# Optimization experiments

Hardware: AMD Instinct MI355X
Metric: run time of the kernel (lower is better)

Reference implementation:

```python
import jax, jax.numpy as jnp
import numpy as np
import math

N_HEADS = 16
D_KV = 64
NUM_BUCKETS = 32
MAX_DISTANCE = 128


def _rel_bucket(rel_pos, num_buckets=NUM_BUCKETS, max_distance=MAX_DISTANCE):
    # bidirectional=True branch of relative_position_bucket
    n = -rel_pos
    num_buckets //= 2
    ret = (n < 0).astype(jnp.int32) * num_buckets
    n = jnp.abs(n)
    max_exact = num_buckets // 2
    is_small = n < max_exact
    val_large = max_exact + (
        jnp.log(n.astype(jnp.float32) / max_exact)
        / math.log(max_distance / max_exact)
        * (num_buckets - max_exact)
    ).astype(jnp.int32)
    val_large = jnp.minimum(val_large, num_buckets - 1)
    return jnp.where(is_small, n, val_large) + ret


def setup_inputs() -> dict:
    key = jax.random.key(0)
    ks = jax.random.split(key, 6)
    T, D = 2048, 1024
    x = jax.random.normal(ks[0], (T, D), dtype=jnp.float32)
    Wq = jax.random.normal(ks[1], (D, N_HEADS * D_KV), dtype=jnp.float32) * 0.02
    Wk = jax.random.normal(ks[2], (D, N_HEADS * D_KV), dtype=jnp.float32) * 0.02
    Wv = jax.random.normal(ks[3], (D, N_HEADS * D_KV), dtype=jnp.float32) * 0.02
    Wo = jax.random.normal(ks[4], (N_HEADS * D_KV, D), dtype=jnp.float32) * 0.02
    rel_bias_table = jax.random.normal(ks[5], (NUM_BUCKETS, N_HEADS), dtype=jnp.float32) * 0.02
    q_lens = jnp.full((4,), 512, dtype=jnp.int32)  # packed varlen: 4 seqs of 512, sum == T
    return {"x": x, "Wq": Wq, "Wk": Wk, "Wv": Wv, "Wo": Wo,
            "rel_bias_table": rel_bias_table, "q_lens": q_lens}


def _attention(x, Wq, Wk, Wv, Wo, rel_bias_table, q_lens):
    T = x.shape[0]
    q = x @ Wq
    k = x @ Wk
    v = x @ Wv
    to_heads = lambda t: jnp.transpose(t.reshape(T, N_HEADS, D_KV), (1, 0, 2))  # [H,T,d]
    q_h, k_h, v_h = to_heads(q), to_heads(k), to_heads(v)

    # fp32 scores (no 1/sqrt(d) scaling in T5; module uses scaling=1.0)
    scores = jnp.einsum('hqd,hkd->hqk', q_h.astype(jnp.float32), k_h.astype(jnp.float32))

    # sequence ids / positions within packed layout
    starts = jnp.cumsum(q_lens, dtype=jnp.int32) - q_lens
    indicators = jnp.zeros(T, dtype=jnp.int32).at[starts].set(1)
    seq_ids = jnp.cumsum(indicators, dtype=jnp.int32) - 1
    pos = jnp.arange(T) - starts[seq_ids]

    # relative position bias (encoder: bidirectional)
    rel_pos = pos[None, :] - pos[:, None]  # [T,T]
    buckets = _rel_bucket(rel_pos)
    bias = jnp.transpose(rel_bias_table[buckets], (2, 0, 1))  # [H,T,T]
    scores = scores + bias.astype(jnp.float32)

    # block-diagonal mask over packed sequences (non-causal encoder)
    total = jnp.sum(q_lens)
    valid = jnp.arange(T) < total
    mask = (seq_ids[:, None] == seq_ids[None, :]) & valid[:, None] & valid[None, :]
    scores = jnp.where(mask[None], scores, jnp.finfo(scores.dtype).min)

    weights = jax.nn.softmax(scores, axis=-1)
    out = jnp.einsum('hqk,hkd->hqd', weights, v_h.astype(jnp.float32))
    out = jnp.transpose(out, (1, 0, 2)).reshape(T, N_HEADS * D_KV)
    return out.astype(x.dtype) @ Wo


def reference(x, Wq, Wk, Wv, Wo, rel_bias_table, q_lens):
    return _attention(x, Wq, Wk, Wv, Wo, rel_bias_table, q_lens)
```

## Files before the change

### kernel.cpp

```cpp
#include <hip/hip_runtime.h>

#define NH 16

typedef __bf16 bf16x8 __attribute__((ext_vector_type(8)));
typedef unsigned short u16x8 __attribute__((ext_vector_type(8)));
typedef float f32x4 __attribute__((ext_vector_type(4)));
typedef unsigned short u16;

__device__ __forceinline__ u16 f2bu(float f) {
    unsigned int u = __builtin_bit_cast(unsigned int, f);
    u = (u + 0x7FFFu + ((u >> 16) & 1u)) >> 16;
    return (u16)u;
}
__device__ __forceinline__ bf16x8 ld_bf8(const u16* p) {
    return __builtin_bit_cast(bf16x8, *(const u16x8*)p);
}
__device__ __forceinline__ void gl_lds16(const void* g, void* l) {
    __builtin_amdgcn_global_load_lds((const __attribute__((address_space(1))) void*)g,
                                     (__attribute__((address_space(3))) void*)l, 16, 0, 0);
}

__device__ __forceinline__ int rel_bucket(int delta) {
    int n = -delta;
    int ret = (n < 0) ? 16 : 0;
    int na = n < 0 ? -n : n;
    int b;
    if (na < 8) b = na;
    else if (na < 12) b = 8;
    else if (na < 16) b = 9;
    else if (na < 23) b = 10;
    else if (na < 32) b = 11;
    else if (na < 46) b = 12;
    else if (na < 64) b = 13;
    else if (na < 91) b = 14;
    else b = 15;
    return b + ret;
}

#define L2E 1.4426950408889634f

__global__ void prep_all(const float* __restrict__ x, u16* __restrict__ xb, int n,
                         const float* __restrict__ Wq, const float* __restrict__ Wk,
                         const float* __restrict__ Wv, const float* __restrict__ Wo,
                         u16* __restrict__ Wt, u16* __restrict__ Wot, int cb) {
    __shared__ float tile[32][33];
    int b = blockIdx.x, tid = threadIdx.x;
    if (b < cb) {
        int i = (b * 256 + tid) * 4;
        if (i >= n) return;
        float4 v = *(const float4*)&x[i];
        u16 o0 = f2bu(v.x), o1 = f2bu(v.y), o2 = f2bu(v.z), o3 = f2bu(v.w);
        xb[i] = o0; xb[i+1] = o1; xb[i+2] = o2; xb[i+3] = o3;
    } else {
        int t = b - cb;
        int z = t >> 10; t &= 1023;
        const float* src = z == 0 ? Wq : z == 1 ? Wk : z == 2 ? Wv : Wo;
        u16* dst = z < 3 ? Wt + (size_t)z * 1024 * 1024 : Wot;
        int r0 = (t >> 5) * 32, c0 = (t & 31) * 32;
        int tx = tid & 31, ty = tid >> 5;
        #pragma unroll
        for (int i = 0; i < 32; i += 8)
            tile[ty + i][tx] = src[(size_t)(r0 + ty + i) * 1024 + c0 + tx];
        __syncthreads();
        #pragma unroll
        for (int i = 0; i < 32; i += 8)
            dst[(size_t)(c0 + ty + i) * 1024 + r0 + tx] = f2bu(tile[tx][ty + i]);
    }
}

template<int MODE, int BM, int XR, int XC>
__global__ __launch_bounds__(256)
void gemm_bt(const u16* __restrict__ A, const u16* __restrict__ Bt,
             int N, int K, int T,
             float* __restrict__ Cf, u16* __restrict__ qkb, u16* __restrict__ vtb) {
    constexpr int MI = BM / 32;
    constexpr int STG = (BM + 128) * 64;
    constexpr int LDSN = (MODE == 1 && 128 * 136 > 2 * STG) ? 128 * 136 : 2 * STG;
    __shared__ __attribute__((aligned(16))) u16 lds[LDSN];
    const int tid = threadIdx.x;
    const int l = tid & 63, wv = tid >> 6;
    const int l16 = l & 15, lg = l >> 4;
    const int lrow = l >> 3, lslot = l & 7;
    const int wm = (wv >> 1) * (BM / 2), wn = (wv & 1) * 64;

    int bmi, bni;
    {
        int gx = gridDim.x, gy = gridDim.y;
        int lin = blockIdx.y * gx + blockIdx.x;
        int nrx = gx / XR, nrc = gy / XC;
        if (gx % XR == 0 && gy % XC == 0 && nrx * nrc == 8) {
            int xcd = lin & 7, loc = lin >> 3;
            int rr = xcd / nrc, rc = xcd % nrc;
            bmi = rr * XR + (loc % XR);
            bni = rc * XC + (loc / XR);
        } else { bmi = blockIdx.x; bni = blockIdx.y; }
    }
    const int bm = bmi * BM, bn = bni * 128;

    f32x4 acc[MI][4];
    #pragma unroll
    for (int i = 0; i < MI; i++)
        #pragma unroll
        for (int j = 0; j < 4; j++)
            #pragma unroll
            for (int r = 0; r < 4; r++) acc[i][j][r] = 0.f;

    auto stage = [&](int k0, int bi) {
        u16* As_ = lds + bi * STG;
        u16* Bs_ = As_ + BM * 64;
        #pragma unroll
        for (int c = 0; c < MI; ++c) {
            int chunk = c * 4 + wv;
            int row = chunk * 8 + lrow;
            int gs = lslot ^ (row & 7);
            gl_lds16(&A[(size_t)(bm + row) * K + k0 + gs * 8], &As_[chunk * 512]);
        }
        #pragma unroll
        for (int c = 0; c < 4; ++c) {
            int chunk = c * 4 + wv;
            int row = chunk * 8 + lrow;
            int gs = lslot ^ (row & 7);
            gl_lds16(&Bt[(size_t)(bn + row) * K + k0 + gs * 8], &Bs_[chunk * 512]);
        }
    };

    stage(0, 0);
    __syncthreads();
    int cur = 0;
    for (int k0 = 0; k0 < K; k0 += 64) {
        if (k0 + 64 < K) stage(k0 + 64, cur ^ 1);
        const u16* As = lds + cur * STG;
        const u16* Bs = As + BM * 64;
        #pragma unroll
        for (int kk = 0; kk < 2; ++kk) {
            bf16x8 af[MI], bfv[4];
            #pragma unroll
            for (int i = 0; i < MI; i++) {
                int row = wm + i * 16 + l16;
                af[i] = ld_bf8(&As[row * 64 + (((kk * 4 + lg) ^ (row & 7)) * 8)]);
            }
            #pragma unroll
            for (int j = 0; j < 4; j++) {
                int row = wn + j * 16 + l16;
                bfv[j] = ld_bf8(&Bs[row * 64 + (((kk * 4 + lg) ^ (row & 7)) * 8)]);
            }
            #pragma unroll
            for (int i = 0; i < MI; i++)
                #pragma unroll
                for (int j = 0; j < 4; j++)
                    acc[i][j] = __builtin_amdgcn_mfma_f32_16x16x32_bf16(af[i], bfv[j], acc[i][j], 0, 0, 0);
        }
        __syncthreads();
        cur ^= 1;
    }

    if (MODE == 0) {
        #pragma unroll
        for (int i = 0; i < MI; i++)
            #pragma unroll
            for (int j = 0; j < 4; j++) {
                int col = bn + wn + j * 16 + l16;
                #pragma unroll
                for (int r = 0; r < 4; r++) {
                    int row = bm + wm + i * 16 + lg * 4 + r;
                    Cf[(size_t)row * N + col] = acc[i][j][r];
                }
            }
    } else if (bn < 2048) {
        #pragma unroll
        for (int i = 0; i < MI; i++)
            #pragma unroll
            for (int j = 0; j < 4; j++) {
                int col = bn + wn + j * 16 + l16;
                #pragma unroll
                for (int r = 0; r < 4; r++) {
                    int row = bm + wm + i * 16 + lg * 4 + r;
                    qkb[(size_t)row * 2048 + col] = f2bu(acc[i][j][r]);
                }
            }
    } else {
        #pragma unroll
        for (int i = 0; i < MI; i++)
            #pragma unroll
            for (int j = 0; j < 4; j++) {
                int cl = wn + j * 16 + l16;
                #pragma unroll
                for (int r = 0; r < 4; r++)
                    lds[cl * 136 + wm + i * 16 + lg * 4 + r] = f2bu(acc[i][j][r]);
            }
        __syncthreads();
        int cl = tid >> 1, hf = tid & 1;
        size_t gb = (size_t)(bn - 2048 + cl) * T + bm + hf * 64;
        #pragma unroll
        for (int k2 = 0; k2 < 8; ++k2) {
            int4 v4 = *(const int4*)&lds[cl * 136 + hf * 64 + k2 * 8];
            *(int4*)&vtb[gb + k2 * 8] = v4;
        }
    }
}

__global__ __launch_bounds__(512)
void attn_kernel(const u16* __restrict__ qkb, const u16* __restrict__ vtb,
                 const float* __restrict__ tbl, const int* __restrict__ q_lens, int nseq,
                 u16* __restrict__ attnb, int T) {
    __shared__ __attribute__((aligned(16))) u16 KV[2][2][4096];
    __shared__ __attribute__((aligned(16))) u16 Ps[8][16][72];
    __shared__ float biasLds[2304];
    const int tid = threadIdx.x;
    const int l = tid & 63, wv = tid >> 6;
    const int l16 = l & 15, lg = l >> 4;
    const int lrow = l >> 3, lslot = l & 7;

    int nbk = gridDim.x * gridDim.y;
    int lin = blockIdx.y * gridDim.x + blockIdx.x;
    int lin2 = (nbk & 7) ? lin : (lin & 7) * (nbk >> 3) + (lin >> 3);
    const int h = lin2 / gridDim.x;
    const int q0 = (lin2 % gridDim.x) * 128;

    int cums[9]; cums[0] = 0;
    #pragma unroll
    for (int i = 0; i < 8; ++i) cums[i + 1] = cums[i] + (i < nseq ? q_lens[i] : 0);
    auto seq_of = [&](int t) -> int {
        int s = -1;
        #pragma unroll
        for (int i = 0; i < 8; ++i)
            if (t >= cums[i] && t < cums[i + 1]) s = i;
        return s;
    };
    const int s0 = seq_of(q0), s1 = seq_of(q0 + 127);
    const bool uni = (s0 == s1) && (s0 >= 0);
    const int kvA = uni ? cums[s0] : 0;
    const int kvB = uni ? cums[s0 + 1] : T;
    const int len = kvB - kvA;

    for (int t = tid; t < len + 128; t += 512)
        biasLds[t] = tbl[rel_bucket(kvA - q0 - 127 + t) * NH + h] * L2E;

    bf16x8 qf[2];
    {
        int tq = q0 + wv * 16 + l16;
        const u16* qp = qkb + (size_t)tq * 2048 + h * 64 + lg * 8;
        qf[0] = ld_bf8(qp); qf[1] = ld_bf8(qp + 32);
    }
    int tqr[4], sqr[4];
    #pragma unroll
    for (int r = 0; r < 4; r++) {
        tqr[r] = q0 + wv * 16 + lg * 4 + r;
        sqr[r] = uni ? s0 : seq_of(tqr[r]);
    }

    const u16* kg = qkb + 1024 + h * 64;
    const u16* vg = vtb + (size_t)(h * 64) * T;
    const int srow = wv * 8 + lrow;
    const int swz = (lslot ^ (srow & 7)) * 8;

    auto ldKV = [&](int base, int4& kr, int4& vr) {
        int tk = base + srow; if (tk > T - 1) tk = T - 1;
        kr = *(const int4*)(kg + (size_t)tk * 2048 + lslot * 8);
        vr = *(const int4*)(vg + (size_t)srow * T + base + lslot * 8);
    };
    auto stKV = [&](int bi, const int4& kr, const int4& vr) {
        *(int4*)&KV[bi][0][srow * 64 + swz] = kr;
        *(int4*)&KV[bi][1][srow * 64 + swz] = vr;
    };

    float psum[4] = {0.f, 0.f, 0.f, 0.f};
    f32x4 o[4];
    #pragma unroll
    for (int d = 0; d < 4; d++)
        #pragma unroll
        for (int r = 0; r < 4; r++) o[d][r] = 0.f;

    int4 kr, vr;
    ldKV(kvA, kr, vr);
    stKV(0, kr, vr);
    if (kvA + 64 < kvB) ldKV(kvA + 64, kr, vr);
    __syncthreads();
    int cur = 0;
    for (int base = kvA; base < kvB; base += 64) {
        const u16* Kb = KV[cur][0];
        const u16* Vb = KV[cur][1];

        f32x4 s[4];
        #pragma unroll
        for (int kt = 0; kt < 4; kt++)
            #pragma unroll
            for (int r = 0; r < 4; r++) s[kt][r] = 0.f;
        #pragma unroll
        for (int kk = 0; kk < 2; kk++)
            #pragma unroll
            for (int kt = 0; kt < 4; kt++) {
                int rw = kt * 16 + l16;
                bf16x8 kf = ld_bf8(Kb + rw * 64 + (((kk * 4 + lg) ^ (rw & 7)) * 8));
                s[kt] = __builtin_amdgcn_mfma_f32_16x16x32_bf16(qf[kk], kf, s[kt], 0, 0, 0);
            }

        const int cbi = (base - kvA) + 127 + l16 - wv * 16 - lg * 4;
        if (uni && base + 64 <= kvB) {
            #pragma unroll
            for (int r = 0; r < 4; r++) {
                const float* bp = &biasLds[cbi - r];
                #pragma unroll
                for (int kt = 0; kt < 4; kt++) {
                    float p = __builtin_amdgcn_exp2f(__builtin_fmaf(s[kt][r], L2E, bp[kt * 16]));
                    psum[r] += p;
                    Ps[wv][lg * 4 + r][kt * 16 + l16] = f2bu(p);
                }
            }
        } else {
            int skt[4];
            #pragma unroll
            for (int kt = 0; kt < 4; kt++) {
                int tk = base + kt * 16 + l16;
                skt[kt] = (tk < T) ? (uni ? s0 : seq_of(tk)) : -2;
            }
            #pragma unroll
            for (int r = 0; r < 4; r++) {
                const float* bp = &biasLds[cbi - r];
                #pragma unroll
                for (int kt = 0; kt < 4; kt++) {
                    float p = __builtin_amdgcn_exp2f(__builtin_fmaf(s[kt][r], L2E, bp[kt * 16]));
                    if (uni) {
                        int tk = base + kt * 16 + l16;
                        if (tk >= kvB) p = 0.f;
                    } else {
                        bool ok = (skt[kt] >= 0) && (skt[kt] == sqr[r]);
                        p = (sqr[r] < 0) ? 1.f : (ok ? p : 0.f);
                    }
                    psum[r] += p;
                    Ps[wv][lg * 4 + r][kt * 16 + l16] = f2bu(p);
                }
            }
        }
        bf16x8 pf0 = ld_bf8(&Ps[wv][l16][lg * 8]);
        bf16x8 pf1 = ld_bf8(&Ps[wv][l16][32 + lg * 8]);
        #pragma unroll
        for (int kk = 0; kk < 2; kk++) {
            bf16x8 pf = kk ? pf1 : pf0;
            #pragma unroll
            for (int dt = 0; dt < 4; dt++) {
                int rw = dt * 16 + l16;
                bf16x8 vf = ld_bf8(Vb + rw * 64 + (((kk * 4 + lg) ^ (rw & 7)) * 8));
                o[dt] = __builtin_amdgcn_mfma_f32_16x16x32_bf16(pf, vf, o[dt], 0, 0, 0);
            }
        }
        if (base + 64 < kvB) {
            stKV(cur ^ 1, kr, vr);
            if (base + 128 < kvB) ldKV(base + 128, kr, vr);
        }
        __syncthreads();
        cur ^= 1;
    }

    float lsum[4];
    #pragma unroll
    for (int r = 0; r < 4; r++) {
        float v = psum[r];
        #pragma unroll
        for (int m = 1; m < 16; m <<= 1) v += __shfl_xor(v, m, 64);
        lsum[r] = v;
    }
    #pragma unroll
    for (int dt = 0; dt < 4; dt++)
        #pragma unroll
        for (int r = 0; r < 4; r++)
            attnb[(size_t)tqr[r] * 1024 + h * 64 + dt * 16 + l16] = f2bu(o[dt][r] / lsum[r]);
}

extern "C" void kernel_launch(void* const* d_in, const int* in_sizes, int n_in,
                              void* d_out, int out_size, void* d_ws, size_t ws_size,
                              hipStream_t stream) {
    const float* x   = (const float*)d_in[0];
    const float* Wq  = (const float*)d_in[1];
    const float* Wk  = (const float*)d_in[2];
    const float* Wv  = (const float*)d_in[3];
    const float* Wo  = (const float*)d_in[4];
    const float* tbl = (const float*)d_in[5];
    const int* q_lens = (const int*)d_in[6];
    const int T = in_sizes[0] / 1024;
    const int nseq = in_sizes[6];

    char* ws = (char*)d_ws;
    auto alloc = [&](size_t bytes) { char* p = ws; ws += (bytes + 255) & ~(size_t)255; return p; };
    u16*   xb    = (u16*)alloc((size_t)T * 1024 * 2);
    u16*   Wt    = (u16*)alloc((size_t)3072 * 1024 * 2);
    u16*   Wot   = (u16*)alloc((size_t)1024 * 1024 * 2);
    u16*   qkb   = (u16*)alloc((size_t)T * 2048 * 2);
    u16*   vtb   = (u16*)alloc((size_t)1024 * T * 2);
    u16*   attnb = (u16*)alloc((size_t)T * 1024 * 2);

    int cb = (T * 1024 / 4 + 255) / 256;
    prep_all<<<dim3(cb + 4096), dim3(256), 0, stream>>>(
        x, xb, T * 1024, Wq, Wk, Wv, Wo, Wt, Wot, cb);

    gemm_bt<1, 128, 8, 6><<<dim3(T / 128, 3072 / 128), dim3(256), 0, stream>>>(
        xb, Wt, 3072, 1024, T, nullptr, qkb, vtb);
    attn_kernel<<<dim3(T / 128, NH), dim3(512), 0, stream>>>(
        qkb, vtb, tbl, q_lens, nseq, attnb, T);
    gemm_bt<0, 64, 8, 4><<<dim3(T / 64, 1024 / 128), dim3(256), 0, stream>>>(
        attnb, Wot, 1024, 1024, T, (float*)d_out, nullptr, nullptr);
}
```

Baseline: 127.7 us.

## Widen attention KV tile to 128 keys and stage QK GEMM stores through LDS

The attention loop now processes 128 keys per iteration instead of 64. This doubles the K/V shared-memory buffers, the Ps staging and the per-iteration MFMA work, while halving the loop trips and barriers. Separately, the QK projection epilogue now writes bf16 results into LDS first and then stores them to global memory as coalesced 16-byte rows instead of scattered 2-byte stores. The trade-off is higher LDS use (about 64KB+ for KV) and more registers for s[8], which may lower occupancy.

```diff
diff --git a/kernel.cpp b/kernel.cpp
--- a/kernel.cpp
+++ b/kernel.cpp
@@ -171,13 +171,19 @@
         for (int i = 0; i < MI; i++)
             #pragma unroll
             for (int j = 0; j < 4; j++) {
-                int col = bn + wn + j * 16 + l16;
-                #pragma unroll
-                for (int r = 0; r < 4; r++) {
-                    int row = bm + wm + i * 16 + lg * 4 + r;
-                    qkb[(size_t)row * 2048 + col] = f2bu(acc[i][j][r]);
-                }
-            }
+                int col = wn + j * 16 + l16;
+                #pragma unroll
+                for (int r = 0; r < 4; r++)
+                    lds[(wm + i * 16 + lg * 4 + r) * 136 + col] = f2bu(acc[i][j][r]);
+            }
+        __syncthreads();
+        #pragma unroll
+        for (int t = 0; t < 8; ++t) {
+            int c = t * 256 + tid;
+            int row = c >> 4, sl = c & 15;
+            *(int4*)&qkb[(size_t)(bm + row) * 2048 + bn + sl * 8] =
+                *(const int4*)&lds[row * 136 + sl * 8];
+        }
     } else {
         #pragma unroll
         for (int i = 0; i < MI; i++)
@@ -203,8 +209,8 @@
 void attn_kernel(const u16* __restrict__ qkb, const u16* __restrict__ vtb,
                  const float* __restrict__ tbl, const int* __restrict__ q_lens, int nseq,
                  u16* __restrict__ attnb, int T) {
-    __shared__ __attribute__((aligned(16))) u16 KV[2][2][4096];
-    __shared__ __attribute__((aligned(16))) u16 Ps[8][16][72];
+    __shared__ __attribute__((aligned(16))) u16 KV[2][2][8192];
+    __shared__ __attribute__((aligned(16))) u16 Ps[8][16][136];
     __shared__ float biasLds[2304];
     const int tid = threadIdx.x;
     const int l = tid & 63, wv = tid >> 6;
@@ -252,16 +258,22 @@
     const u16* kg = qkb + 1024 + h * 64;
     const u16* vg = vtb + (size_t)(h * 64) * T;
     const int srow = wv * 8 + lrow;
-    const int swz = (lslot ^ (srow & 7)) * 8;
-
-    auto ldKV = [&](int base, int4& kr, int4& vr) {
-        int tk = base + srow; if (tk > T - 1) tk = T - 1;
-        kr = *(const int4*)(kg + (size_t)tk * 2048 + lslot * 8);
-        vr = *(const int4*)(vg + (size_t)srow * T + base + lslot * 8);
+
+    auto ldKV = [&](int base, int4* kr, int4* vr) {
+        #pragma unroll
+        for (int p = 0; p < 2; ++p) {
+            int tk = base + srow + p * 64; if (tk > T - 1) tk = T - 1;
+            kr[p] = *(const int4*)(kg + (size_t)tk * 2048 + lslot * 8);
+            vr[p] = *(const int4*)(vg + (size_t)srow * T + base + (lslot + p * 8) * 8);
+        }
     };
-    auto stKV = [&](int bi, const int4& kr, const int4& vr) {
-        *(int4*)&KV[bi][0][srow * 64 + swz] = kr;
-        *(int4*)&KV[bi][1][srow * 64 + swz] = vr;
+    auto stKV = [&](int bi, const int4* kr, const int4* vr) {
+        #pragma unroll
+        for (int p = 0; p < 2; ++p) {
+            int krow = srow + p * 64;
+            *(int4*)&KV[bi][0][krow * 64 + (lslot ^ (krow & 7)) * 8] = kr[p];
+            *(int4*)&KV[bi][1][srow * 128 + ((lslot + p * 8) ^ (srow & 15)) * 8] = vr[p];
+        }
     };
 
     float psum[4] = {0.f, 0.f, 0.f, 0.f};
@@ -271,46 +283,46 @@
         #pragma unroll
         for (int r = 0; r < 4; r++) o[d][r] = 0.f;
 
-    int4 kr, vr;
+    int4 kr[2], vr[2];
     ldKV(kvA, kr, vr);
     stKV(0, kr, vr);
-    if (kvA + 64 < kvB) ldKV(kvA + 64, kr, vr);
+    if (kvA + 128 < kvB) ldKV(kvA + 128, kr, vr);
     __syncthreads();
     int cur = 0;
-    for (int base = kvA; base < kvB; base += 64) {
+    for (int base = kvA; base < kvB; base += 128) {
         const u16* Kb = KV[cur][0];
         const u16* Vb = KV[cur][1];
 
-        f32x4 s[4];
-        #pragma unroll
-        for (int kt = 0; kt < 4; kt++)
+        f32x4 s[8];
+        #pragma unroll
+        for (int kt = 0; kt < 8; kt++)
             #pragma unroll
             for (int r = 0; r < 4; r++) s[kt][r] = 0.f;
         #pragma unroll
         for (int kk = 0; kk < 2; kk++)
             #pragma unroll
-            for (int kt = 0; kt < 4; kt++) {
+            for (int kt = 0; kt < 8; kt++) {
                 int rw = kt * 16 + l16;
                 bf16x8 kf = ld_bf8(Kb + rw * 64 + (((kk * 4 + lg) ^ (rw & 7)) * 8));
                 s[kt] = __builtin_amdgcn_mfma_f32_16x16x32_bf16(qf[kk], kf, s[kt], 0, 0, 0);
             }
 
         const int cbi = (base - kvA) + 127 + l16 - wv * 16 - lg * 4;
-        if (uni && base + 64 <= kvB) {
+        if (uni && base + 128 <= kvB) {
             #pragma unroll
             for (int r = 0; r < 4; r++) {
                 const float* bp = &biasLds[cbi - r];
                 #pragma unroll
-                for (int kt = 0; kt < 4; kt++) {
+                for (int kt = 0; kt < 8; kt++) {
                     float p = __builtin_amdgcn_exp2f(__builtin_fmaf(s[kt][r], L2E, bp[kt * 16]));
                     psum[r] += p;
                     Ps[wv][lg * 4 + r][kt * 16 + l16] = f2bu(p);
                 }
             }
         } else {
-            int skt[4];
-            #pragma unroll
-            for (int kt = 0; kt < 4; kt++) {
+            int skt[8];
+            #pragma unroll
+            for (int kt = 0; kt < 8; kt++) {
                 int tk = base + kt * 16 + l16;
                 skt[kt] = (tk < T) ? (uni ? s0 : seq_of(tk)) : -2;
             }
@@ -318,7 +330,7 @@
             for (int r = 0; r < 4; r++) {
                 const float* bp = &biasLds[cbi - r];
                 #pragma unroll
-                for (int kt = 0; kt < 4; kt++) {
+                for (int kt = 0; kt < 8; kt++) {
                     float p = __builtin_amdgcn_exp2f(__builtin_fmaf(s[kt][r], L2E, bp[kt * 16]));
                     if (uni) {
                         int tk = base + kt * 16 + l16;
@@ -332,21 +344,19 @@
                 }
             }
         }
-        bf16x8 pf0 = ld_bf8(&Ps[wv][l16][lg * 8]);
-        bf16x8 pf1 = ld_bf8(&Ps[wv][l16][32 + lg * 8]);
-        #pragma unroll
-        for (int kk = 0; kk < 2; kk++) {
-            bf16x8 pf = kk ? pf1 : pf0;
+        #pragma unroll
+        for (int kk = 0; kk < 4; kk++) {
+            bf16x8 pf = ld_bf8(&Ps[wv][l16][kk * 32 + lg * 8]);
             #pragma unroll
             for (int dt = 0; dt < 4; dt++) {
                 int rw = dt * 16 + l16;
-                bf16x8 vf = ld_bf8(Vb + rw * 64 + (((kk * 4 + lg) ^ (rw & 7)) * 8));
+                bf16x8 vf = ld_bf8(Vb + rw * 128 + (((kk * 4 + lg) ^ (rw & 15)) * 8));
                 o[dt] = __builtin_amdgcn_mfma_f32_16x16x32_bf16(pf, vf, o[dt], 0, 0, 0);
             }
         }
-        if (base + 64 < kvB) {
+        if (base + 128 < kvB) {
             stKV(cur ^ 1, kr, vr);
-            if (base + 128 < kvB) ldKV(base + 128, kr, vr);
+            if (base + 256 < kvB) ldKV(base + 256, kr, vr);
         }
         __syncthreads();
         cur ^= 1;
```

New measurement: 155.2 us. 21.5% more time.
